# Kernel tuning notes

Measured on AMD Instinct MI355X. Metric: run time of the kernel, lower is better.

Reference implementation:

```python
import jax, jax.numpy as jnp
import numpy as np

N, E, S, D, FIN, FE, L = 250000, 1000000, 1000, 64, 16, 8, 3


def layernorm(x, g, b):
    mu = jnp.mean(x, axis=-1, keepdims=True)
    var = jnp.var(x, axis=-1, keepdims=True)
    return (x - mu) * jax.lax.rsqrt(var + 1e-5) * g + b


def mlp(x, W1, b1, W2, b2):
    return jax.nn.relu(x @ W1 + b1) @ W2 + b2


def _fwd(x, edge_attr, W_init, b_init,
         lu_We, lu_be, lu_eps, lu_W1, lu_b1, lu_W2, lu_b2, lu_g, lu_bn,
         vv_eps, vv_W1, vv_b1, vv_W2, vv_b2, vv_g, vv_bn,
         vu_eps, vu_W1, vu_b1, vu_W2, vu_b2, vu_g, vu_bn,
         gl_eps, gl_W1, gl_b1, gl_W2, gl_b2, gl_g, gl_bn,
         W_jk, b_jk,
         edge_index, node_idx, root_idx, transpose_idx):
    src, dst = edge_index[0], edge_index[1]
    h = x @ W_init + b_init  # init_encoder -> [N, D]
    cnt = jnp.maximum(
        jax.ops.segment_sum(jnp.ones((x.shape[0], 1), h.dtype), node_idx, num_segments=S), 1.0)
    for l in range(L):
        # lu: local message passing in each subgraph (GINE-style gnn_layer + norm)
        e_emb = edge_attr @ lu_We[l] + lu_be[l]  # edge encoder [E, D]
        msg = jax.nn.relu(h[src] + e_emb)
        agg = jax.ops.segment_sum(msg, dst, num_segments=h.shape[0])
        h_lu = layernorm(mlp((1.0 + lu_eps[l]) * h + agg,
                             lu_W1[l], lu_b1[l], lu_W2[l], lu_b2[l]), lu_g[l], lu_bn[l])
        # vv: root tuple of each subgraph broadcast back to its members
        h_vv = layernorm(mlp((1.0 + vv_eps[l]) * h + h[root_idx][node_idx],
                             vv_W1[l], vv_b1[l], vv_W2[l], vv_b2[l]), vv_g[l], vv_bn[l])
        # vu: transposed-tuple gather
        h_vu = layernorm(mlp((1.0 + vu_eps[l]) * h + h[transpose_idx],
                             vu_W1[l], vu_b1[l], vu_W2[l], vu_b2[l]), vu_g[l], vu_bn[l])
        # global: subgraph mean pooling broadcast back
        g = jax.ops.segment_sum(h, node_idx, num_segments=S) / cnt
        h_gl = layernorm(mlp((1.0 + gl_eps[l]) * h + g[node_idx],
                             gl_W1[l], gl_b1[l], gl_W2[l], gl_b2[l]), gl_g[l], gl_bn[l])
        h = h_lu + h_vv + h_vu + h_gl  # dropout=identity (eval), residual=False
    pooled = jax.ops.segment_sum(h, node_idx, num_segments=S)  # SV pooling
    return pooled @ W_jk + b_jk  # JK='last' decoder -> [S, D]


def setup_inputs():
    key = jax.random.key(0)
    ks = jax.random.split(key, 20)
    sc = 0.1
    rn = lambda k, shp: jax.random.normal(k, shp, jnp.float32) * sc
    z = lambda shp: jnp.zeros(shp, jnp.float32)
    o = lambda shp: jnp.ones(shp, jnp.float32)
    return {
        "x": jax.random.normal(ks[0], (N, FIN), jnp.float32),
        "edge_attr": jax.random.normal(ks[1], (E, FE), jnp.float32),
        "edge_index": jax.random.randint(ks[2], (2, E), 0, N),
        "node_idx": jax.random.randint(ks[3], (N,), 0, S),
        "root_idx": jax.random.randint(ks[4], (S,), 0, N),
        "transpose_idx": jax.random.randint(ks[5], (N,), 0, N),
        "W_init": rn(ks[6], (FIN, D)), "b_init": z((D,)),
        "lu_We": rn(ks[7], (L, FE, D)), "lu_be": z((L, D)),
        "lu_eps": z((L,)),
        "lu_W1": rn(ks[8], (L, D, D)), "lu_b1": z((L, D)),
        "lu_W2": rn(ks[9], (L, D, D)), "lu_b2": z((L, D)),
        "lu_g": o((L, D)), "lu_bn": z((L, D)),
        "vv_eps": z((L,)),
        "vv_W1": rn(ks[10], (L, D, D)), "vv_b1": z((L, D)),
        "vv_W2": rn(ks[11], (L, D, D)), "vv_b2": z((L, D)),
        "vv_g": o((L, D)), "vv_bn": z((L, D)),
        "vu_eps": z((L,)),
        "vu_W1": rn(ks[12], (L, D, D)), "vu_b1": z((L, D)),
        "vu_W2": rn(ks[13], (L, D, D)), "vu_b2": z((L, D)),
        "vu_g": o((L, D)), "vu_bn": z((L, D)),
        "gl_eps": z((L,)),
        "gl_W1": rn(ks[14], (L, D, D)), "gl_b1": z((L, D)),
        "gl_W2": rn(ks[15], (L, D, D)), "gl_b2": z((L, D)),
        "gl_g": o((L, D)), "gl_bn": z((L, D)),
        "W_jk": rn(ks[16], (D, D)), "b_jk": z((D,)),
    }


def reference(x, edge_attr, edge_index, node_idx, root_idx, transpose_idx,
              W_init, b_init,
              lu_We, lu_be, lu_eps, lu_W1, lu_b1, lu_W2, lu_b2, lu_g, lu_bn,
              vv_eps, vv_W1, vv_b1, vv_W2, vv_b2, vv_g, vv_bn,
              vu_eps, vu_W1, vu_b1, vu_W2, vu_b2, vu_g, vu_bn,
              gl_eps, gl_W1, gl_b1, gl_W2, gl_b2, gl_g, gl_bn,
              W_jk, b_jk):
    return _fwd(x, edge_attr, W_init, b_init,
                lu_We, lu_be, lu_eps, lu_W1, lu_b1, lu_W2, lu_b2, lu_g, lu_bn,
                vv_eps, vv_W1, vv_b1, vv_W2, vv_b2, vv_g, vv_bn,
                vu_eps, vu_W1, vu_b1, vu_W2, vu_b2, vu_g, vu_bn,
                gl_eps, gl_W1, gl_b1, gl_W2, gl_b2, gl_g, gl_bn,
                W_jk, b_jk,
                edge_index, node_idx, root_idx, transpose_idx)
```

## Files before the change

kernel.cpp:

```cpp
#include <hip/hip_runtime.h>

#define NN 250000
#define EE 1000000
#define SS 1000
#define DD 64
#define FIN 16
#define FEE 8
#define NL 3
#define LDH 72
#define SCHUNK 1024
#define SNB ((NN + SCHUNK - 1) / SCHUNK)
#define EB (NN / 4)

typedef __attribute__((ext_vector_type(8))) short bf16x8;
typedef __attribute__((ext_vector_type(4))) float f32x4;

static __device__ __forceinline__ short f2bf(float f) {
  union { float f; unsigned u; } v{f};
  unsigned r = (v.u + 0x7fffu + ((v.u >> 16) & 1u)) >> 16;
  return (short)r;
}
static __device__ __forceinline__ float bfl(unsigned u) {
  union { unsigned u; float f; } v{u << 16};
  return v.f;
}
static __device__ __forceinline__ float bfh(unsigned u) {
  union { unsigned u; float f; } v{u & 0xffff0000u};
  return v.f;
}
static __device__ __forceinline__ float bfu(unsigned short u) {
  union { unsigned u; float f; } v{(unsigned)u << 16};
  return v.f;
}
static __device__ __forceinline__ unsigned pack2(float a, float b) {
  return (unsigned)(unsigned short)f2bf(a) | ((unsigned)(unsigned short)f2bf(b) << 16);
}
static __device__ __forceinline__ void unp8(uint4 v, float* o) {
  o[0] = bfl(v.x); o[1] = bfh(v.x); o[2] = bfl(v.y); o[3] = bfh(v.y);
  o[4] = bfl(v.z); o[5] = bfh(v.z); o[6] = bfl(v.w); o[7] = bfh(v.w);
}

__global__ __launch_bounds__(256) void k_hist(const int* __restrict__ idx,
                                              int* __restrict__ cnt, int n) {
  int i = blockIdx.x * 256 + threadIdx.x;
  if (i < n) atomicAdd(&cnt[idx[i]], 1);
}

__global__ __launch_bounds__(256) void k_scan1(const int* __restrict__ cntv,
                                               int* __restrict__ off,
                                               int* __restrict__ curs,
                                               int* __restrict__ bsums, int n) {
  __shared__ int ls[256];
  int b = blockIdx.x, t = threadIdx.x;
  int base = b * SCHUNK + t * 4;
  int v[4];
#pragma unroll
  for (int j = 0; j < 4; j++) v[j] = (base + j < n) ? cntv[base + j] : 0;
  int s4 = v[0] + v[1] + v[2] + v[3];
  ls[t] = s4;
  __syncthreads();
  for (int o = 1; o < 256; o <<= 1) {
    int x = (t >= o) ? ls[t - o] : 0;
    __syncthreads();
    ls[t] += x;
    __syncthreads();
  }
  int run = ls[t] - s4;
#pragma unroll
  for (int j = 0; j < 4; j++) {
    if (base + j < n) { off[base + j] = run; curs[base + j] = run; }
    run += v[j];
  }
  if (t == 255) bsums[b] = ls[255];
}

__global__ __launch_bounds__(256) void k_scan2(int* __restrict__ bsums, int nb) {
  __shared__ int ls[256];
  int t = threadIdx.x;
  int v = (t < nb) ? bsums[t] : 0;
  ls[t] = v;
  __syncthreads();
  for (int o = 1; o < 256; o <<= 1) {
    int x = (t >= o) ? ls[t - o] : 0;
    __syncthreads();
    ls[t] += x;
    __syncthreads();
  }
  if (t < nb) bsums[t] = ls[t] - v;
}

__global__ __launch_bounds__(256) void k_scan3(int* __restrict__ off,
                                               int* __restrict__ curs,
                                               const int* __restrict__ bsums, int n) {
  int b = blockIdx.x, t = threadIdx.x;
  int add = bsums[b];
  int base = b * SCHUNK + t * 4;
#pragma unroll
  for (int j = 0; j < 4; j++)
    if (base + j < n) { off[base + j] += add; curs[base + j] += add; }
}

__global__ __launch_bounds__(256) void k_bucket_e(const int* __restrict__ src,
                                                  const int* __restrict__ dst,
                                                  const float* __restrict__ ea,
                                                  int* __restrict__ curs,
                                                  int* __restrict__ ssrc,
                                                  unsigned short* __restrict__ eas) {
  int e = blockIdx.x * 256 + threadIdx.x;
  if (e >= EE) return;
  int pos = atomicAdd(&curs[dst[e]], 1);
  ssrc[pos] = src[e];
  const float* a = &ea[(size_t)e * 8];
  uint4 p;
  p.x = pack2(a[0], a[1]);
  p.y = pack2(a[2], a[3]);
  p.z = pack2(a[4], a[5]);
  p.w = pack2(a[6], a[7]);
  *(uint4*)&eas[(size_t)pos * 8] = p;
}

__global__ __launch_bounds__(256) void k_bucket_n(const int* __restrict__ nidx,
                                                  int* __restrict__ curs,
                                                  int* __restrict__ nsorted) {
  int n = blockIdx.x * 256 + threadIdx.x;
  if (n >= NN) return;
  int pos = atomicAdd(&curs[nidx[n]], 1);
  nsorted[pos] = n;
}

__global__ __launch_bounds__(256) void k_cinv(const int* __restrict__ ncnt,
                                              float* __restrict__ cinv) {
  int s = blockIdx.x * 256 + threadIdx.x;
  if (s < SS) {
    float c = (float)ncnt[s];
    cinv[s] = 1.0f / (c < 1.0f ? 1.0f : c);
  }
}

__global__ __launch_bounds__(256) void k_init(const float* __restrict__ x,
                                              const float* __restrict__ W,
                                              const float* __restrict__ b,
                                              unsigned short* __restrict__ hb) {
  int gid = blockIdx.x * 256 + threadIdx.x;
  int n = gid >> 6, d = gid & 63;
  const float* xr = x + (size_t)n * FIN;
  float acc = b[d];
#pragma unroll
  for (int k = 0; k < FIN; k++) acc += xr[k] * W[k * DD + d];
  hb[gid] = (unsigned short)f2bf(acc);
}

struct WPrep { const float* W[8]; };

__global__ __launch_bounds__(256) void k_wprep(WPrep P, short* __restrict__ wbt) {
  int gid = blockIdx.x * 256 + threadIdx.x;
  int slot = gid >> 12;
  int e = gid & 4095;
  int n = e >> 6, k = e & 63;
  int bg = slot / NL, l = slot % NL;
  float v = P.W[bg][(size_t)l * 4096 + k * 64 + n];
  wbt[gid] = f2bf(v);
}

struct ProdArgs {
  const unsigned short* hb;
  const unsigned short* eas;
  const int* ssrc;
  const int* eoff;
  const int* ecnt;
  const float* We;
  const float* be;
  unsigned short* aggb;
  const int* nsorted;
  const int* noff;
  const int* ncnt;
  const float* cinv;
  unsigned short* gsumb;
};

__global__ __launch_bounds__(256) void k_prod(ProdArgs P) {
  __shared__ float red[256];
  int tid = threadIdx.x;
  int blk = blockIdx.x;
  if (blk < EB) {
    int v = blk * 4 + (tid >> 6);
    int d = tid & 63;
    float w[8];
#pragma unroll
    for (int k = 0; k < 8; k++) w[k] = P.We[k * 64 + d];
    float bed = P.be[d];
    int base = P.eoff[v], deg = P.ecnt[v];
    float acc = 0.0f;
    int i = 0;
    for (; i + 4 <= deg; i += 4) {
      int s0 = P.ssrc[base + i + 0];
      int s1 = P.ssrc[base + i + 1];
      int s2 = P.ssrc[base + i + 2];
      int s3 = P.ssrc[base + i + 3];
      unsigned short g0 = P.hb[(size_t)s0 * 64 + d];
      unsigned short g1 = P.hb[(size_t)s1 * 64 + d];
      unsigned short g2 = P.hb[(size_t)s2 * 64 + d];
      unsigned short g3 = P.hb[(size_t)s3 * 64 + d];
      uint4 a0 = *(const uint4*)&P.eas[(size_t)(base + i + 0) * 8];
      uint4 a1 = *(const uint4*)&P.eas[(size_t)(base + i + 1) * 8];
      uint4 a2 = *(const uint4*)&P.eas[(size_t)(base + i + 2) * 8];
      uint4 a3 = *(const uint4*)&P.eas[(size_t)(base + i + 3) * 8];
      float e0 = bed + bfl(a0.x) * w[0] + bfh(a0.x) * w[1] + bfl(a0.y) * w[2] + bfh(a0.y) * w[3] +
                 bfl(a0.z) * w[4] + bfh(a0.z) * w[5] + bfl(a0.w) * w[6] + bfh(a0.w) * w[7];
      float e1 = bed + bfl(a1.x) * w[0] + bfh(a1.x) * w[1] + bfl(a1.y) * w[2] + bfh(a1.y) * w[3] +
                 bfl(a1.z) * w[4] + bfh(a1.z) * w[5] + bfl(a1.w) * w[6] + bfh(a1.w) * w[7];
      float e2 = bed + bfl(a2.x) * w[0] + bfh(a2.x) * w[1] + bfl(a2.y) * w[2] + bfh(a2.y) * w[3] +
                 bfl(a2.z) * w[4] + bfh(a2.z) * w[5] + bfl(a2.w) * w[6] + bfh(a2.w) * w[7];
      float e3 = bed + bfl(a3.x) * w[0] + bfh(a3.x) * w[1] + bfl(a3.y) * w[2] + bfh(a3.y) * w[3] +
                 bfl(a3.z) * w[4] + bfh(a3.z) * w[5] + bfl(a3.w) * w[6] + bfh(a3.w) * w[7];
      float m0 = bfu(g0) + e0;
      float m1 = bfu(g1) + e1;
      float m2 = bfu(g2) + e2;
      float m3 = bfu(g3) + e3;
      acc += (m0 > 0.0f ? m0 : 0.0f) + (m1 > 0.0f ? m1 : 0.0f) +
             (m2 > 0.0f ? m2 : 0.0f) + (m3 > 0.0f ? m3 : 0.0f);
    }
    for (; i < deg; i++) {
      int s0 = P.ssrc[base + i];
      unsigned short g0 = P.hb[(size_t)s0 * 64 + d];
      uint4 a0 = *(const uint4*)&P.eas[(size_t)(base + i) * 8];
      float e0 = bed + bfl(a0.x) * w[0] + bfh(a0.x) * w[1] + bfl(a0.y) * w[2] + bfh(a0.y) * w[3] +
                 bfl(a0.z) * w[4] + bfh(a0.z) * w[5] + bfl(a0.w) * w[6] + bfh(a0.w) * w[7];
      float m0 = bfu(g0) + e0;
      acc += m0 > 0.0f ? m0 : 0.0f;
    }
    P.aggb[(size_t)v * 64 + d] = (unsigned short)f2bf(acc);
  } else {
    int s = blk - EB;
    int ch = tid & 63, r = tid >> 6;
    int base = P.noff[s], c = P.ncnt[s];
    float acc = 0.0f;
    int i = r;
    for (; i + 12 < c; i += 16) {
      int n0 = P.nsorted[base + i];
      int n1 = P.nsorted[base + i + 4];
      int n2 = P.nsorted[base + i + 8];
      int n3 = P.nsorted[base + i + 12];
      acc += bfu(P.hb[(size_t)n0 * 64 + ch]) + bfu(P.hb[(size_t)n1 * 64 + ch]) +
             bfu(P.hb[(size_t)n2 * 64 + ch]) + bfu(P.hb[(size_t)n3 * 64 + ch]);
    }
    for (; i < c; i += 4) acc += bfu(P.hb[(size_t)P.nsorted[base + i] * 64 + ch]);
    red[tid] = acc;
    __syncthreads();
    if (r == 0) {
      float vsum = red[ch] + red[64 + ch] + red[128 + ch] + red[192 + ch];
      P.gsumb[s * 64 + ch] = (unsigned short)f2bf(vsum * P.cinv[s]);
    }
  }
}

struct NodeArgs {
  const unsigned short* hb;
  const unsigned short* aggb;
  const unsigned short* gsumb;
  const int* nidx;
  const int* root;
  const int* tr;
  const float* eps[4];
  const short* wt1[4];
  const short* wt2[4];
  const float* b1[4];
  const float* b2[4];
  const float* ga[4];
  const float* bb[4];
  unsigned short* hbout;
};

__global__ __launch_bounds__(256, 4) void k_node(NodeArgs A) {
  __shared__ short sT[4][16 * LDH];
  int tid = threadIdx.x;
  int wv = tid >> 6;
  int lane = tid & 63;
  int m = lane & 15, q = lane >> 4;
  int gm = blockIdx.x * 64 + wv * 16 + m;
  bool valid = gm < NN;
  if (!valid) gm = 0;
  short* band = &sT[wv][0];

  int s = A.nidx[gm];
  int rv = A.root[s];
  int rt = A.tr[gm];

  const unsigned short* hrow = &A.hb[(size_t)gm * 64];
  uint4 hq0 = *(const uint4*)&hrow[q * 8];
  uint4 hq1 = *(const uint4*)&hrow[32 + q * 8];
  float hv[8], hw[8];
  unp8(hq0, hv);
  unp8(hq1, hw);

  float hacc[4][4];
#pragma unroll
  for (int i = 0; i < 4; i++)
#pragma unroll
    for (int j = 0; j < 4; j++) hacc[i][j] = 0.0f;

#pragma unroll
  for (int b = 0; b < 4; b++) {
    float aeps = 1.0f + A.eps[b][0];
    uint4 o0, o1;
    if (b == 0) {
      const unsigned short* r0 = &A.aggb[(size_t)gm * 64];
      o0 = *(const uint4*)&r0[q * 8];
      o1 = *(const uint4*)&r0[32 + q * 8];
    } else if (b == 1) {
      const unsigned short* r0 = &A.hb[(size_t)rv * 64];
      o0 = *(const uint4*)&r0[q * 8];
      o1 = *(const uint4*)&r0[32 + q * 8];
    } else if (b == 2) {
      const unsigned short* r0 = &A.hb[(size_t)rt * 64];
      o0 = *(const uint4*)&r0[q * 8];
      o1 = *(const uint4*)&r0[32 + q * 8];
    } else {
      const unsigned short* r0 = &A.gsumb[(size_t)s * 64];
      o0 = *(const uint4*)&r0[q * 8];
      o1 = *(const uint4*)&r0[32 + q * 8];
    }
    float ov[8], ow[8];
    unp8(o0, ov);
    unp8(o1, ow);

    union { bf16x8 v; uint4 u; } a0u, a1u;
    a0u.u.x = pack2(aeps * hv[0] + ov[0], aeps * hv[1] + ov[1]);
    a0u.u.y = pack2(aeps * hv[2] + ov[2], aeps * hv[3] + ov[3]);
    a0u.u.z = pack2(aeps * hv[4] + ov[4], aeps * hv[5] + ov[5]);
    a0u.u.w = pack2(aeps * hv[6] + ov[6], aeps * hv[7] + ov[7]);
    a1u.u.x = pack2(aeps * hw[0] + ow[0], aeps * hw[1] + ow[1]);
    a1u.u.y = pack2(aeps * hw[2] + ow[2], aeps * hw[3] + ow[3]);
    a1u.u.z = pack2(aeps * hw[4] + ow[4], aeps * hw[5] + ow[5]);
    a1u.u.w = pack2(aeps * hw[6] + ow[6], aeps * hw[7] + ow[7]);

    const short* w1 = A.wt1[b];
    const short* w2 = A.wt2[b];
    const float* b1p = A.b1[b];
    const float* b2p = A.b2[b];

#pragma unroll
    for (int t = 0; t < 4; t++) {
      int n = t * 16 + m;
      bf16x8 w0 = *(const bf16x8*)&w1[n * 64 + q * 8];
      bf16x8 wk = *(const bf16x8*)&w1[n * 64 + 32 + q * 8];
      float bv = b1p[n];
      f32x4 c = {bv, bv, bv, bv};
      c = __builtin_amdgcn_mfma_f32_16x16x32_bf16(a0u.v, w0, c, 0, 0, 0);
      c = __builtin_amdgcn_mfma_f32_16x16x32_bf16(a1u.v, wk, c, 0, 0, 0);
#pragma unroll
      for (int r = 0; r < 4; r++) {
        float v = c[r];
        v = v > 0.0f ? v : 0.0f;
        band[(q * 4 + r) * LDH + n] = f2bf(v);
      }
    }

    bf16x8 t0 = *(const bf16x8*)&band[m * LDH + q * 8];
    bf16x8 t1 = *(const bf16x8*)&band[m * LDH + 32 + q * 8];

    f32x4 c2[4];
#pragma unroll
    for (int t = 0; t < 4; t++) {
      int n = t * 16 + m;
      bf16x8 w0 = *(const bf16x8*)&w2[n * 64 + q * 8];
      bf16x8 wk = *(const bf16x8*)&w2[n * 64 + 32 + q * 8];
      float bv = b2p[n];
      f32x4 c = {bv, bv, bv, bv};
      c = __builtin_amdgcn_mfma_f32_16x16x32_bf16(t0, w0, c, 0, 0, 0);
      c = __builtin_amdgcn_mfma_f32_16x16x32_bf16(t1, wk, c, 0, 0, 0);
      c2[t] = c;
    }

    const float* ga = A.ga[b];
    const float* bbp = A.bb[b];
    float gav[4], bbv[4];
#pragma unroll
    for (int t = 0; t < 4; t++) {
      gav[t] = ga[t * 16 + m];
      bbv[t] = bbp[t * 16 + m];
    }
#pragma unroll
    for (int r = 0; r < 4; r++) {
      float s1 = c2[0][r] + c2[1][r] + c2[2][r] + c2[3][r];
      float s2 = c2[0][r] * c2[0][r] + c2[1][r] * c2[1][r] +
                 c2[2][r] * c2[2][r] + c2[3][r] * c2[3][r];
#pragma unroll
      for (int o = 1; o < 16; o <<= 1) {
        s1 += __shfl_xor(s1, o);
        s2 += __shfl_xor(s2, o);
      }
      float mu = s1 * (1.0f / 64.0f);
      float var = s2 * (1.0f / 64.0f) - mu * mu;
      float rr = rsqrtf(var + 1e-5f);
#pragma unroll
      for (int t = 0; t < 4; t++)
        hacc[r][t] += (c2[t][r] - mu) * rr * gav[t] + bbv[t];
    }
  }

#pragma unroll
  for (int r = 0; r < 4; r++)
#pragma unroll
    for (int t = 0; t < 4; t++)
      band[(q * 4 + r) * LDH + t * 16 + m] = f2bf(hacc[r][t]);
  if (valid) {
    uint4 v0 = *(const uint4*)&band[m * LDH + q * 8];
    uint4 v1 = *(const uint4*)&band[m * LDH + 32 + q * 8];
    unsigned short* orow = &A.hbout[(size_t)gm * 64];
    *(uint4*)&orow[q * 8] = v0;
    *(uint4*)&orow[32 + q * 8] = v1;
  }
}

__global__ __launch_bounds__(256) void k_pool_out(const unsigned short* __restrict__ hb,
                                                  const int* __restrict__ nsorted,
                                                  const int* __restrict__ noff,
                                                  const int* __restrict__ ncnt,
                                                  const float* __restrict__ W,
                                                  const float* __restrict__ bjk,
                                                  float* __restrict__ out) {
  __shared__ float red[256];
  __shared__ float pr[64];
  int s = blockIdx.x, tid = threadIdx.x;
  int ch = tid & 63, r = tid >> 6;
  int base = noff[s], c = ncnt[s];
  float acc = 0.0f;
  int i = r;
  for (; i + 12 < c; i += 16) {
    int n0 = nsorted[base + i];
    int n1 = nsorted[base + i + 4];
    int n2 = nsorted[base + i + 8];
    int n3 = nsorted[base + i + 12];
    acc += bfu(hb[(size_t)n0 * 64 + ch]) + bfu(hb[(size_t)n1 * 64 + ch]) +
           bfu(hb[(size_t)n2 * 64 + ch]) + bfu(hb[(size_t)n3 * 64 + ch]);
  }
  for (; i < c; i += 4) acc += bfu(hb[(size_t)nsorted[base + i] * 64 + ch]);
  red[tid] = acc;
  __syncthreads();
  if (r == 0) pr[ch] = red[ch] + red[64 + ch] + red[128 + ch] + red[192 + ch];
  __syncthreads();
  if (tid < 64) {
    float o = bjk[tid];
#pragma unroll 8
    for (int k = 0; k < 64; k++) o += pr[k] * W[k * 64 + tid];
    out[s * 64 + tid] = o;
  }
}

extern "C" void kernel_launch(void* const* d_in, const int* in_sizes, int n_in,
                              void* d_out, int out_size, void* d_ws, size_t ws_size,
                              hipStream_t stream) {
  const float* x = (const float*)d_in[0];
  const float* edge_attr = (const float*)d_in[1];
  const int* edge_index = (const int*)d_in[2];
  const int* node_idx = (const int*)d_in[3];
  const int* root_idx = (const int*)d_in[4];
  const int* transpose_idx = (const int*)d_in[5];
  const float* W_init = (const float*)d_in[6];
  const float* b_init = (const float*)d_in[7];
  const float* lu_We = (const float*)d_in[8];
  const float* lu_be = (const float*)d_in[9];
  const float* eps_[4] = {(const float*)d_in[10], (const float*)d_in[17],
                          (const float*)d_in[24], (const float*)d_in[31]};
  const float* W1_[4] = {(const float*)d_in[11], (const float*)d_in[18],
                         (const float*)d_in[25], (const float*)d_in[32]};
  const float* b1_[4] = {(const float*)d_in[12], (const float*)d_in[19],
                         (const float*)d_in[26], (const float*)d_in[33]};
  const float* W2_[4] = {(const float*)d_in[13], (const float*)d_in[20],
                         (const float*)d_in[27], (const float*)d_in[34]};
  const float* b2_[4] = {(const float*)d_in[14], (const float*)d_in[21],
                         (const float*)d_in[28], (const float*)d_in[35]};
  const float* ga_[4] = {(const float*)d_in[15], (const float*)d_in[22],
                         (const float*)d_in[29], (const float*)d_in[36]};
  const float* bn_[4] = {(const float*)d_in[16], (const float*)d_in[23],
                         (const float*)d_in[30], (const float*)d_in[37]};
  const float* W_jk = (const float*)d_in[38];
  const float* b_jk = (const float*)d_in[39];

  char* p = (char*)d_ws;
  auto carve = [&](size_t bytes) -> char* {
    char* r = p;
    p += (bytes + 255) & ~(size_t)255;
    return r;
  };
  unsigned short* hb0 = (unsigned short*)carve((size_t)NN * DD * 2);
  unsigned short* hb1 = (unsigned short*)carve((size_t)NN * DD * 2);
  unsigned short* aggb = (unsigned short*)carve((size_t)NN * DD * 2);
  unsigned short* gsumb = (unsigned short*)carve(SS * DD * 2);
  float* cinv = (float*)carve(SS * 4);
  short* wbt = (short*)carve(24 * 4096 * 2);
  int* ecnt = (int*)carve(NN * 4);
  int* eoff = (int*)carve(NN * 4);
  int* ecurs = (int*)carve(NN * 4);
  int* ebsum = (int*)carve(256 * 4);
  int* ssrc = (int*)carve((size_t)EE * 4);
  unsigned short* eas = (unsigned short*)carve((size_t)EE * FEE * 2);
  int* ncnt = (int*)carve(SS * 4);
  int* noff = (int*)carve(SS * 4);
  int* ncurs = (int*)carve(SS * 4);
  int* nbsum = (int*)carve(256 * 4);
  int* nsorted = (int*)carve(NN * 4);

  const int* srcp = edge_index;
  const int* dstp = edge_index + EE;

  hipMemsetAsync(ecnt, 0, NN * 4, stream);
  hipMemsetAsync(ncnt, 0, SS * 4, stream);
  k_hist<<<(EE + 255) / 256, 256, 0, stream>>>(dstp, ecnt, EE);
  k_hist<<<(NN + 255) / 256, 256, 0, stream>>>(node_idx, ncnt, NN);
  k_scan1<<<SNB, 256, 0, stream>>>(ecnt, eoff, ecurs, ebsum, NN);
  k_scan2<<<1, 256, 0, stream>>>(ebsum, SNB);
  k_scan3<<<SNB, 256, 0, stream>>>(eoff, ecurs, ebsum, NN);
  k_scan1<<<1, 256, 0, stream>>>(ncnt, noff, ncurs, nbsum, SS);
  k_bucket_e<<<(EE + 255) / 256, 256, 0, stream>>>(srcp, dstp, edge_attr, ecurs, ssrc, eas);
  k_bucket_n<<<(NN + 255) / 256, 256, 0, stream>>>(node_idx, ncurs, nsorted);
  k_cinv<<<(SS + 255) / 256, 256, 0, stream>>>(ncnt, cinv);

  k_init<<<(NN * DD) / 256, 256, 0, stream>>>(x, W_init, b_init, hb0);

  WPrep P;
  for (int b = 0; b < 4; b++) {
    P.W[b * 2 + 0] = W1_[b];
    P.W[b * 2 + 1] = W2_[b];
  }
  k_wprep<<<(24 * 4096) / 256, 256, 0, stream>>>(P, wbt);

  unsigned short* hbc = hb0;
  unsigned short* hbn = hb1;
  for (int l = 0; l < NL; l++) {
    ProdArgs PR;
    PR.hb = hbc; PR.eas = eas; PR.ssrc = ssrc; PR.eoff = eoff; PR.ecnt = ecnt;
    PR.We = lu_We + (size_t)l * FEE * DD;
    PR.be = lu_be + l * DD;
    PR.aggb = aggb;
    PR.nsorted = nsorted; PR.noff = noff; PR.ncnt = ncnt; PR.cinv = cinv;
    PR.gsumb = gsumb;
    k_prod<<<EB + SS, 256, 0, stream>>>(PR);

    NodeArgs A;
    A.hb = hbc; A.aggb = aggb; A.gsumb = gsumb;
    A.nidx = node_idx; A.root = root_idx; A.tr = transpose_idx;
    for (int b = 0; b < 4; b++) {
      A.eps[b] = eps_[b] + l;
      A.wt1[b] = wbt + ((size_t)(b * 2 + 0) * NL + l) * 4096;
      A.wt2[b] = wbt + ((size_t)(b * 2 + 1) * NL + l) * 4096;
      A.b1[b] = b1_[b] + l * DD;
      A.b2[b] = b2_[b] + l * DD;
      A.ga[b] = ga_[b] + l * DD;
      A.bb[b] = bn_[b] + l * DD;
    }
    A.hbout = hbn;
    k_node<<<(NN + 63) / 64, 256, 0, stream>>>(A);
    unsigned short* tmpb = hbc; hbc = hbn; hbn = tmpb;
  }

  k_pool_out<<<SS, 256, 0, stream>>>(hbc, nsorted, noff, ncnt, W_jk, b_jk, (float*)d_out);
}
```

Baseline: 1.316 ms.

## Fuse edge aggregation into node kernel via shared-memory band

```diff
diff --git a/kernel.cpp b/kernel.cpp
--- a/kernel.cpp
+++ b/kernel.cpp
@@ -10,7 +10,6 @@
 #define LDH 72
 #define SCHUNK 1024
 #define SNB ((NN + SCHUNK - 1) / SCHUNK)
-#define EB (NN / 4)
 
 typedef __attribute__((ext_vector_type(8))) short bf16x8;
 typedef __attribute__((ext_vector_type(4))) float f32x4;
@@ -162,102 +161,45 @@
   wbt[gid] = f2bf(v);
 }
 
-struct ProdArgs {
+__global__ __launch_bounds__(256) void k_gmean(const unsigned short* __restrict__ hb,
+                                               const int* __restrict__ nsorted,
+                                               const int* __restrict__ noff,
+                                               const int* __restrict__ ncnt,
+                                               const float* __restrict__ cinv,
+                                               unsigned short* __restrict__ gsumb) {
+  __shared__ float red[256];
+  int s = blockIdx.x;
+  int tid = threadIdx.x;
+  int ch = tid & 63, r = tid >> 6;
+  int base = noff[s], c = ncnt[s];
+  float acc = 0.0f;
+  int i = r;
+  for (; i + 12 < c; i += 16) {
+    int n0 = nsorted[base + i];
+    int n1 = nsorted[base + i + 4];
+    int n2 = nsorted[base + i + 8];
+    int n3 = nsorted[base + i + 12];
+    acc += bfu(hb[(size_t)n0 * 64 + ch]) + bfu(hb[(size_t)n1 * 64 + ch]) +
+           bfu(hb[(size_t)n2 * 64 + ch]) + bfu(hb[(size_t)n3 * 64 + ch]);
+  }
+  for (; i < c; i += 4) acc += bfu(hb[(size_t)nsorted[base + i] * 64 + ch]);
+  red[tid] = acc;
+  __syncthreads();
+  if (r == 0) {
+    float vsum = red[ch] + red[64 + ch] + red[128 + ch] + red[192 + ch];
+    gsumb[s * 64 + ch] = (unsigned short)f2bf(vsum * cinv[s]);
+  }
+}
+
+struct NodeArgs {
   const unsigned short* hb;
+  const unsigned short* gsumb;
   const unsigned short* eas;
   const int* ssrc;
   const int* eoff;
   const int* ecnt;
   const float* We;
   const float* be;
-  unsigned short* aggb;
-  const int* nsorted;
-  const int* noff;
-  const int* ncnt;
-  const float* cinv;
-  unsigned short* gsumb;
-};
-
-__global__ __launch_bounds__(256) void k_prod(ProdArgs P) {
-  __shared__ float red[256];
-  int tid = threadIdx.x;
-  int blk = blockIdx.x;
-  if (blk < EB) {
-    int v = blk * 4 + (tid >> 6);
-    int d = tid & 63;
-    float w[8];
-#pragma unroll
-    for (int k = 0; k < 8; k++) w[k] = P.We[k * 64 + d];
-    float bed = P.be[d];
-    int base = P.eoff[v], deg = P.ecnt[v];
-    float acc = 0.0f;
-    int i = 0;
-    for (; i + 4 <= deg; i += 4) {
-      int s0 = P.ssrc[base + i + 0];
-      int s1 = P.ssrc[base + i + 1];
-      int s2 = P.ssrc[base + i + 2];
-      int s3 = P.ssrc[base + i + 3];
-      unsigned short g0 = P.hb[(size_t)s0 * 64 + d];
-      unsigned short g1 = P.hb[(size_t)s1 * 64 + d];
-      unsigned short g2 = P.hb[(size_t)s2 * 64 + d];
-      unsigned short g3 = P.hb[(size_t)s3 * 64 + d];
-      uint4 a0 = *(const uint4*)&P.eas[(size_t)(base + i + 0) * 8];
-      uint4 a1 = *(const uint4*)&P.eas[(size_t)(base + i + 1) * 8];
-      uint4 a2 = *(const uint4*)&P.eas[(size_t)(base + i + 2) * 8];
-      uint4 a3 = *(const uint4*)&P.eas[(size_t)(base + i + 3) * 8];
-      float e0 = bed + bfl(a0.x) * w[0] + bfh(a0.x) * w[1] + bfl(a0.y) * w[2] + bfh(a0.y) * w[3] +
-                 bfl(a0.z) * w[4] + bfh(a0.z) * w[5] + bfl(a0.w) * w[6] + bfh(a0.w) * w[7];
-      float e1 = bed + bfl(a1.x) * w[0] + bfh(a1.x) * w[1] + bfl(a1.y) * w[2] + bfh(a1.y) * w[3] +
-                 bfl(a1.z) * w[4] + bfh(a1.z) * w[5] + bfl(a1.w) * w[6] + bfh(a1.w) * w[7];
-      float e2 = bed + bfl(a2.x) * w[0] + bfh(a2.x) * w[1] + bfl(a2.y) * w[2] + bfh(a2.y) * w[3] +
-                 bfl(a2.z) * w[4] + bfh(a2.z) * w[5] + bfl(a2.w) * w[6] + bfh(a2.w) * w[7];
-      float e3 = bed + bfl(a3.x) * w[0] + bfh(a3.x) * w[1] + bfl(a3.y) * w[2] + bfh(a3.y) * w[3] +
-                 bfl(a3.z) * w[4] + bfh(a3.z) * w[5] + bfl(a3.w) * w[6] + bfh(a3.w) * w[7];
-      float m0 = bfu(g0) + e0;
-      float m1 = bfu(g1) + e1;
-      float m2 = bfu(g2) + e2;
-      float m3 = bfu(g3) + e3;
-      acc += (m0 > 0.0f ? m0 : 0.0f) + (m1 > 0.0f ? m1 : 0.0f) +
-             (m2 > 0.0f ? m2 : 0.0f) + (m3 > 0.0f ? m3 : 0.0f);
-    }
-    for (; i < deg; i++) {
-      int s0 = P.ssrc[base + i];
-      unsigned short g0 = P.hb[(size_t)s0 * 64 + d];
-      uint4 a0 = *(const uint4*)&P.eas[(size_t)(base + i) * 8];
-      float e0 = bed + bfl(a0.x) * w[0] + bfh(a0.x) * w[1] + bfl(a0.y) * w[2] + bfh(a0.y) * w[3] +
-                 bfl(a0.z) * w[4] + bfh(a0.z) * w[5] + bfl(a0.w) * w[6] + bfh(a0.w) * w[7];
-      float m0 = bfu(g0) + e0;
-      acc += m0 > 0.0f ? m0 : 0.0f;
-    }
-    P.aggb[(size_t)v * 64 + d] = (unsigned short)f2bf(acc);
-  } else {
-    int s = blk - EB;
-    int ch = tid & 63, r = tid >> 6;
-    int base = P.noff[s], c = P.ncnt[s];
-    float acc = 0.0f;
-    int i = r;
-    for (; i + 12 < c; i += 16) {
-      int n0 = P.nsorted[base + i];
-      int n1 = P.nsorted[base + i + 4];
-      int n2 = P.nsorted[base + i + 8];
-      int n3 = P.nsorted[base + i + 12];
-      acc += bfu(P.hb[(size_t)n0 * 64 + ch]) + bfu(P.hb[(size_t)n1 * 64 + ch]) +
-             bfu(P.hb[(size_t)n2 * 64 + ch]) + bfu(P.hb[(size_t)n3 * 64 + ch]);
-    }
-    for (; i < c; i += 4) acc += bfu(P.hb[(size_t)P.nsorted[base + i] * 64 + ch]);
-    red[tid] = acc;
-    __syncthreads();
-    if (r == 0) {
-      float vsum = red[ch] + red[64 + ch] + red[128 + ch] + red[192 + ch];
-      P.gsumb[s * 64 + ch] = (unsigned short)f2bf(vsum * P.cinv[s]);
-    }
-  }
-}
-
-struct NodeArgs {
-  const unsigned short* hb;
-  const unsigned short* aggb;
-  const unsigned short* gsumb;
   const int* nidx;
   const int* root;
   const int* tr;
@@ -277,10 +219,64 @@
   int wv = tid >> 6;
   int lane = tid & 63;
   int m = lane & 15, q = lane >> 4;
-  int gm = blockIdx.x * 64 + wv * 16 + m;
+  int row0 = blockIdx.x * 64 + wv * 16;
+  int gm = row0 + m;
   bool valid = gm < NN;
   if (!valid) gm = 0;
   short* band = &sT[wv][0];
+
+  {
+    int d = lane;
+    float w[8];
+#pragma unroll
+    for (int k = 0; k < 8; k++) w[k] = A.We[k * 64 + d];
+    float bed = A.be[d];
+    for (int rr = 0; rr < 16; rr++) {
+      int v = row0 + rr;
+      if (v >= NN) v = 0;
+      int base = A.eoff[v], deg = A.ecnt[v];
+      float acc = 0.0f;
+      int i = 0;
+      for (; i + 4 <= deg; i += 4) {
+        int s0 = A.ssrc[base + i + 0];
+        int s1 = A.ssrc[base + i + 1];
+        int s2 = A.ssrc[base + i + 2];
+        int s3 = A.ssrc[base + i + 3];
+        unsigned short g0 = A.hb[(size_t)s0 * 64 + d];
+        unsigned short g1 = A.hb[(size_t)s1 * 64 + d];
+        unsigned short g2 = A.hb[(size_t)s2 * 64 + d];
+        unsigned short g3 = A.hb[(size_t)s3 * 64 + d];
+        uint4 a0 = *(const uint4*)&A.eas[(size_t)(base + i + 0) * 8];
+        uint4 a1 = *(const uint4*)&A.eas[(size_t)(base + i + 1) * 8];
+        uint4 a2 = *(const uint4*)&A.eas[(size_t)(base + i + 2) * 8];
+        uint4 a3 = *(const uint4*)&A.eas[(size_t)(base + i + 3) * 8];
+        float e0 = bed + bfl(a0.x) * w[0] + bfh(a0.x) * w[1] + bfl(a0.y) * w[2] + bfh(a0.y) * w[3] +
+                   bfl(a0.z) * w[4] + bfh(a0.z) * w[5] + bfl(a0.w) * w[6] + bfh(a0.w) * w[7];
+        float e1 = bed + bfl(a1.x) * w[0] + bfh(a1.x) * w[1] + bfl(a1.y) * w[2] + bfh(a1.y) * w[3] +
+                   bfl(a1.z) * w[4] + bfh(a1.z) * w[5] + bfl(a1.w) * w[6] + bfh(a1.w) * w[7];
+        float e2 = bed + bfl(a2.x) * w[0] + bfh(a2.x) * w[1] + bfl(a2.y) * w[2] + bfh(a2.y) * w[3] +
+                   bfl(a2.z) * w[4] + bfh(a2.z) * w[5] + bfl(a2.w) * w[6] + bfh(a2.w) * w[7];
+        float e3 = bed + bfl(a3.x) * w[0] + bfh(a3.x) * w[1] + bfl(a3.y) * w[2] + bfh(a3.y) * w[3] +
+                   bfl(a3.z) * w[4] + bfh(a3.z) * w[5] + bfl(a3.w) * w[6] + bfh(a3.w) * w[7];
+        float m0 = bfu(g0) + e0;
+        float m1 = bfu(g1) + e1;
+        float m2 = bfu(g2) + e2;
+        float m3 = bfu(g3) + e3;
+        acc += (m0 > 0.0f ? m0 : 0.0f) + (m1 > 0.0f ? m1 : 0.0f) +
+               (m2 > 0.0f ? m2 : 0.0f) + (m3 > 0.0f ? m3 : 0.0f);
+      }
+      for (; i < deg; i++) {
+        int s0 = A.ssrc[base + i];
+        unsigned short g0 = A.hb[(size_t)s0 * 64 + d];
+        uint4 a0 = *(const uint4*)&A.eas[(size_t)(base + i) * 8];
+        float e0 = bed + bfl(a0.x) * w[0] + bfh(a0.x) * w[1] + bfl(a0.y) * w[2] + bfh(a0.y) * w[3] +
+                   bfl(a0.z) * w[4] + bfh(a0.z) * w[5] + bfl(a0.w) * w[6] + bfh(a0.w) * w[7];
+        float m0 = bfu(g0) + e0;
+        acc += m0 > 0.0f ? m0 : 0.0f;
+      }
+      band[rr * LDH + d] = f2bf(acc);
+    }
+  }
 
   int s = A.nidx[gm];
   int rv = A.root[s];
@@ -302,27 +298,21 @@
 #pragma unroll
   for (int b = 0; b < 4; b++) {
     float aeps = 1.0f + A.eps[b][0];
-    uint4 o0, o1;
+    float ov[8], ow[8];
     if (b == 0) {
-      const unsigned short* r0 = &A.aggb[(size_t)gm * 64];
-      o0 = *(const uint4*)&r0[q * 8];
-      o1 = *(const uint4*)&r0[32 + q * 8];
-    } else if (b == 1) {
-      const unsigned short* r0 = &A.hb[(size_t)rv * 64];
-      o0 = *(const uint4*)&r0[q * 8];
-      o1 = *(const uint4*)&r0[32 + q * 8];
-    } else if (b == 2) {
-      const unsigned short* r0 = &A.hb[(size_t)rt * 64];
-      o0 = *(const uint4*)&r0[q * 8];
-      o1 = *(const uint4*)&r0[32 + q * 8];
+      uint4 o0 = *(const uint4*)&band[m * LDH + q * 8];
+      uint4 o1 = *(const uint4*)&band[m * LDH + 32 + q * 8];
+      unp8(o0, ov);
+      unp8(o1, ow);
     } else {
-      const unsigned short* r0 = &A.gsumb[(size_t)s * 64];
-      o0 = *(const uint4*)&r0[q * 8];
-      o1 = *(const uint4*)&r0[32 + q * 8];
-    }
-    float ov[8], ow[8];
-    unp8(o0, ov);
-    unp8(o1, ow);
+      const unsigned short* r0 = (b == 1) ? &A.hb[(size_t)rv * 64]
+                               : (b == 2) ? &A.hb[(size_t)rt * 64]
+                                          : &A.gsumb[(size_t)s * 64];
+      uint4 o0 = *(const uint4*)&r0[q * 8];
+      uint4 o1 = *(const uint4*)&r0[32 + q * 8];
+      unp8(o0, ov);
+      unp8(o1, ow);
+    }
 
     union { bf16x8 v; uint4 u; } a0u, a1u;
     a0u.u.x = pack2(aeps * hv[0] + ov[0], aeps * hv[1] + ov[1]);
@@ -486,7 +476,6 @@
   };
   unsigned short* hb0 = (unsigned short*)carve((size_t)NN * DD * 2);
   unsigned short* hb1 = (unsigned short*)carve((size_t)NN * DD * 2);
-  unsigned short* aggb = (unsigned short*)carve((size_t)NN * DD * 2);
   unsigned short* gsumb = (unsigned short*)carve(SS * DD * 2);
   float* cinv = (float*)carve(SS * 4);
   short* wbt = (short*)carve(24 * 4096 * 2);
@@ -529,17 +518,13 @@
   unsigned short* hbc = hb0;
   unsigned short* hbn = hb1;
   for (int l = 0; l < NL; l++) {
-    ProdArgs PR;
-    PR.hb = hbc; PR.eas = eas; PR.ssrc = ssrc; PR.eoff = eoff; PR.ecnt = ecnt;
-    PR.We = lu_We + (size_t)l * FEE * DD;
-    PR.be = lu_be + l * DD;
-    PR.aggb = aggb;
-    PR.nsorted = nsorted; PR.noff = noff; PR.ncnt = ncnt; PR.cinv = cinv;
-    PR.gsumb = gsumb;
-    k_prod<<<EB + SS, 256, 0, stream>>>(PR);
+    k_gmean<<<SS, 256, 0, stream>>>(hbc, nsorted, noff, ncnt, cinv, gsumb);
 
     NodeArgs A;
-    A.hb = hbc; A.aggb = aggb; A.gsumb = gsumb;
+    A.hb = hbc; A.gsumb = gsumb;
+    A.eas = eas; A.ssrc = ssrc; A.eoff = eoff; A.ecnt = ecnt;
+    A.We = lu_We + (size_t)l * FEE * DD;
+    A.be = lu_be + l * DD;
     A.nidx = node_idx; A.root = root_idx; A.tr = transpose_idx;
     for (int b = 0; b < 4; b++) {
       A.eps[b] = eps_[b] + l;
```

Result: faster. 1.203 ms (-8.6%).
